# Kernel optimization log

Hardware: AMD Instinct MI355X
Metric: run time of the kernel (lower is better)

The kernel has to match this reference:

```python
import jax, jax.numpy as jnp
import numpy as np

ALPHA = 0.2  # LeakyReLU negative slope
N = 1024     # num_particles
DIM = 3
F_IN = 2 * DIM   # 6
NH = 64          # n_hidden_features
H = 4            # n_heads
T = 12


def _gat_attend(feat, a_vec, slope):
    # feat: (..., N, K); a_vec: (..., 2K) split into source/dest halves
    k = feat.shape[-1]
    f_src = jnp.einsum('...nk,...k->...n', feat, a_vec[..., :k])
    f_dst = jnp.einsum('...nk,...k->...n', feat, a_vec[..., k:])
    e = jax.nn.leaky_relu(f_src[..., :, None] + f_dst[..., None, :], slope)
    attn = jax.nn.softmax(e, axis=-1)  # (..., N, N) dense particle attention
    return jnp.einsum('...ij,...jk->...ik', attn, feat)


def pat_layer(x, W_heads, a_heads, W_out, a_out):
    # x: (N, F_IN); W_heads: (H, F_IN, NH); a_heads: (H, 2*NH)
    # W_out: (H*NH, F_OUT); a_out: (2*F_OUT)
    hW = jnp.einsum('nf,hfk->hnk', x, W_heads)          # (H, N, NH)
    heads = jax.nn.elu(_gat_attend(hW, a_heads, ALPHA))  # (H, N, NH)
    x2 = heads.transpose(1, 0, 2).reshape(x.shape[0], -1)  # (N, H*NH) concat
    hW2 = x2 @ W_out                                     # (N, F_OUT)
    return _gat_attend(hW2, a_out, ALPHA)                # output head, no elu


def setup_inputs() -> dict:
    key = jax.random.key(0)
    ks = jax.random.split(key, 13)
    s = 0.1
    d = {'states': jax.random.normal(ks[0], (T, N, F_IN), jnp.float32)}
    names = ['Wx', 'ax', 'Wxo', 'axo', 'Wh', 'ah', 'Who', 'aho', 'Wy', 'ay', 'Wyo', 'ayo']
    shapes = [(H, F_IN, NH), (H, 2 * NH), (H * NH, F_IN), (2 * F_IN)] * 3
    for i, (nm, sh) in enumerate(zip(names, shapes)):
        sh = sh if isinstance(sh, tuple) else (sh,)
        d[nm] = s * jax.random.normal(ks[i + 1], sh, jnp.float32)
    return d


def reference(states, Wx, ax, Wxo, axo, Wh, ah, Who, aho, Wy, ay, Wyo, ayo):
    def step(h_prev, x_t):
        h_t = pat_layer(x_t, Wx, ax, Wxo, axo) + pat_layer(h_prev, Wh, ah, Who, aho)
        y_t = x_t + pat_layer(h_t, Wy, ay, Wyo, ayo)
        return h_t, y_t

    h0 = jnp.zeros((N, F_IN), states.dtype)
    _, ys = jax.lax.scan(step, h0, states)
    return ys  # (T, N, 2*dim)
```

## Files before the change

kernel.cpp:

```cpp
#include <hip/hip_runtime.h>
#include <hip/hip_bf16.h>

#define ALPHA 0.2f

typedef float v2f __attribute__((ext_vector_type(2)));
typedef short bf16x8 __attribute__((ext_vector_type(8)));
typedef float f32x4 __attribute__((ext_vector_type(4)));

__device__ __forceinline__ float wsum(float v){
  #pragma unroll
  for (int m = 1; m < 64; m <<= 1) v += __shfl_xor(v, m, 64);
  return v;
}
__device__ __forceinline__ float wmax(float v){
  #pragma unroll
  for (int m = 1; m < 64; m <<= 1) v = fmaxf(v, __shfl_xor(v, m, 64));
  return v;
}

__global__ void k_detect(const unsigned short* __restrict__ s, int n, int* __restrict__ flag){
  int i = blockIdx.x * 256 + threadIdx.x;
  if (i < n){
    unsigned short u = s[i];
    if ((u & 0x7F80u) == 0x7F80u) atomicOr(flag, 1);
  }
}

struct Ptr13 { const void* p[13]; };
__global__ void k_cvtAll(Ptr13 src, float* __restrict__ xs, float* __restrict__ wsW,
                         const int* __restrict__ flag){
  const int n = blockIdx.x * 256 + threadIdx.x;
  const int F = *flag;
  if (n < 73728){
    xs[n] = F ? ((const float*)src.p[0])[n]
              : __bfloat162float(((const __hip_bfloat16*)src.p[0])[n]);
    return;
  }
  const int m = n - 73728;
  if (m >= 10788) return;
  const int segend[12] = {1536,2048,3584,3596,5132,5644,7180,7192,8728,9240,10776,10788};
  const int dstoff[12] = {0,1536,2048,3584,3600,5136,5648,7184,7200,8736,9248,10784};
  int seg = 0;
  #pragma unroll
  for (int i = 0; i < 12; ++i) if (m >= segend[i]) seg = i + 1;
  const int local = m - (seg ? segend[seg - 1] : 0);
  float v;
  if (F) v = ((const float*)src.p[seg + 1])[local];
  else   v = __bfloat162float(((const __hip_bfloat16*)src.p[seg + 1])[local]);
  wsW[dstoff[seg] + local] = v;
}

__launch_bounds__(256)
__global__ void k_prepT(const float* __restrict__ X, const float* __restrict__ W,
                        const float* __restrict__ a,
                        __hip_bfloat16* __restrict__ Vt, float* __restrict__ fsd)
{
  __shared__ float WS[384];
  __shared__ float aS[128];
  __shared__ __align__(16) __hip_bfloat16 tileT[64 * 264];
  const int t = threadIdx.x;
  const int b = blockIdx.y;
  const int h = blockIdx.z;
  const int row0 = blockIdx.x * 256;
  const int row = row0 + t;
  for (int i = t; i < 384; i += 256) WS[i] = W[h * 384 + i];
  if (t < 128) aS[t] = a[h * 128 + t];
  __syncthreads();
  float x[6];
  const float* xp = X + ((size_t)b * 1024 + row) * 6;
  #pragma unroll
  for (int f = 0; f < 6; ++f) x[f] = xp[f];
  float fs = 0.f, fd = 0.f;
  for (int k = 0; k < 64; ++k){
    float v = 0.f;
    #pragma unroll
    for (int f = 0; f < 6; ++f) v += x[f] * WS[f * 64 + k];
    fs += v * aS[k]; fd += v * aS[64 + k];
    tileT[k * 264 + t] = __float2bfloat16(v);
  }
  fsd[(((size_t)b * 4 + h) * 2 + 0) * 1024 + row] = fs;
  fsd[(((size_t)b * 4 + h) * 2 + 1) * 1024 + row] = fd;
  __syncthreads();
  const int k = t >> 2, seg = t & 3;
  __hip_bfloat16* dst = Vt + (((size_t)b * 4 + h) * 64 + k) * 1032 + row0 + seg * 64;
  const __hip_bfloat16* src = tileT + k * 264 + seg * 64;
  #pragma unroll
  for (int i = 0; i < 8; ++i)
    ((uint4*)dst)[i] = ((const uint4*)src)[i];
}

__launch_bounds__(256)
__global__ void k_attM(const __hip_bfloat16* __restrict__ Vt, const float* __restrict__ fsd,
                       const float* __restrict__ Wout, const float* __restrict__ aout,
                       float* __restrict__ hW2part, float* __restrict__ f2part)
{
  const int h = blockIdx.x & 3;
  const int row0 = (blockIdx.x >> 2) * 64;
  const int b = blockIdx.y;
  const int t = threadIdx.x;
  const int wv = t >> 6, lane = t & 63;
  const int n = lane & 15, q = lane >> 4;
  const size_t bh = (size_t)b * 4 + h;

  __shared__ float dS[1024];
  __shared__ float WoS[384];
  __shared__ float aoS[12];
  __shared__ float redW[4];

  const float* fb = fsd + bh * 2048;
  float4 dv = *(const float4*)(fb + 1024 + t * 4);
  for (int i = t; i < 384; i += 256) WoS[i] = Wout[h * 384 + i];
  if (t < 12) aoS[t] = aout[t];
  *(float4*)&dS[t * 4] = dv;
  const float sW = fb[row0 + wv * 16 + n];
  float lm = fmaxf(fmaxf(dv.x, dv.y), fmaxf(dv.z, dv.w));
  lm = wmax(lm);
  if (lane == 0) redW[wv] = lm;
  __syncthreads();
  const float maxd = fmaxf(fmaxf(redW[0], redW[1]), fmaxf(redW[2], redW[3]));
  float mW = sW + maxd; mW = fmaxf(mW, ALPHA * mW);

  const __hip_bfloat16* vbase = Vt + (bh * 64 + n) * 1032 + q * 8;
  f32x4 acc[4];
  #pragma unroll
  for (int nt = 0; nt < 4; ++nt) acc[nt] = (f32x4){0.f, 0.f, 0.f, 0.f};
  float den = 0.f;

  for (int jt = 0; jt < 16; ++jt){
    bf16x8 b0[4], b1[4];
    #pragma unroll
    for (int nt = 0; nt < 4; ++nt){
      b0[nt] = *(const bf16x8*)(vbase + nt * 16512 + jt * 64);
      b1[nt] = *(const bf16x8*)(vbase + nt * 16512 + jt * 64 + 32);
    }
    const float* dp = &dS[jt * 64 + q * 8];
    float d0[8], d1[8];
    *(float4*)&d0[0] = *(const float4*)(dp);
    *(float4*)&d0[4] = *(const float4*)(dp + 4);
    *(float4*)&d1[0] = *(const float4*)(dp + 32);
    *(float4*)&d1[4] = *(const float4*)(dp + 36);
    bf16x8 a0, a1;
    #pragma unroll
    for (int i = 0; i < 8; ++i){
      float e0 = sW + d0[i]; e0 = fmaxf(e0, ALPHA * e0);
      __hip_bfloat16 w0 = __float2bfloat16(__expf(fminf(e0 - mW, 0.f)));
      a0[i] = __builtin_bit_cast(short, w0);
      den += __bfloat162float(w0);
      float e1 = sW + d1[i]; e1 = fmaxf(e1, ALPHA * e1);
      __hip_bfloat16 w1 = __float2bfloat16(__expf(fminf(e1 - mW, 0.f)));
      a1[i] = __builtin_bit_cast(short, w1);
      den += __bfloat162float(w1);
    }
    #pragma unroll
    for (int nt = 0; nt < 4; ++nt)
      acc[nt] = __builtin_amdgcn_mfma_f32_16x16x32_bf16(a0, b0[nt], acc[nt], 0, 0, 0);
    #pragma unroll
    for (int nt = 0; nt < 4; ++nt)
      acc[nt] = __builtin_amdgcn_mfma_f32_16x16x32_bf16(a1, b1[nt], acc[nt], 0, 0, 0);
  }
  den += __shfl_xor(den, 16, 64);
  den += __shfl_xor(den, 32, 64);

  float o[4][6];
  #pragma unroll
  for (int reg = 0; reg < 4; ++reg)
    #pragma unroll
    for (int f = 0; f < 6; ++f) o[reg][f] = 0.f;
  #pragma unroll
  for (int reg = 0; reg < 4; ++reg){
    const float dn = __shfl(den, q * 4 + reg, 64);
    #pragma unroll
    for (int nt = 0; nt < 4; ++nt){
      float v = acc[nt][reg] / dn;
      v = v > 0.f ? v : (__expf(v) - 1.f);
      #pragma unroll
      for (int f = 0; f < 6; ++f) o[reg][f] += v * WoS[(nt * 16 + n) * 6 + f];
    }
  }
  #pragma unroll
  for (int mm = 1; mm < 16; mm <<= 1)
    #pragma unroll
    for (int reg = 0; reg < 4; ++reg)
      #pragma unroll
      for (int f = 0; f < 6; ++f) o[reg][f] += __shfl_xor(o[reg][f], mm, 64);
  if (n == 0){
    #pragma unroll
    for (int reg = 0; reg < 4; ++reg){
      const int row = row0 + wv * 16 + q * 4 + reg;
      float* hp = hW2part + bh * 6144 + row * 6;
      float fs = 0.f, fd = 0.f;
      #pragma unroll
      for (int f = 0; f < 6; ++f){
        hp[f] = o[reg][f];
        fs += o[reg][f] * aoS[f]; fd += o[reg][f] * aoS[6 + f];
      }
      f2part[bh * 2048 + row]        = fs;
      f2part[bh * 2048 + 1024 + row] = fd;
    }
  }
}

__launch_bounds__(256)
__global__ void k_attP(const __hip_bfloat16* __restrict__ VtP, const float* __restrict__ fsd,
                       const float* __restrict__ Wout, const float* __restrict__ aout,
                       float* __restrict__ hW2part, float* __restrict__ f2part)
{
  const int h = blockIdx.x & 3;
  const int row0 = (blockIdx.x >> 2) * 16;
  const int t = threadIdx.x;
  const int wv = t >> 6, lane = t & 63;
  const int n = lane & 15, q = lane >> 4;

  __shared__ float dS[1024];
  __shared__ float WoS[384];
  __shared__ float aoS[12];
  __shared__ float redW[4];
  __shared__ float accS[4][16][65];
  __shared__ float denP[4][16];

  const float* fb = fsd + (size_t)h * 2048;
  float4 dv = *(const float4*)(fb + 1024 + t * 4);
  for (int i = t; i < 384; i += 256) WoS[i] = Wout[h * 384 + i];
  if (t < 12) aoS[t] = aout[t];
  *(float4*)&dS[t * 4] = dv;
  const float sW = fb[row0 + n];
  float lm = fmaxf(fmaxf(dv.x, dv.y), fmaxf(dv.z, dv.w));
  lm = wmax(lm);
  if (lane == 0) redW[wv] = lm;
  __syncthreads();
  const float maxd = fmaxf(fmaxf(redW[0], redW[1]), fmaxf(redW[2], redW[3]));
  float mW = sW + maxd; mW = fmaxf(mW, ALPHA * mW);

  const __hip_bfloat16* vbase = VtP + ((size_t)h * 64 + n) * 1024 + q * 8;
  f32x4 acc[4];
  #pragma unroll
  for (int nt = 0; nt < 4; ++nt) acc[nt] = (f32x4){0.f, 0.f, 0.f, 0.f};
  float den = 0.f;

  #pragma unroll
  for (int u = 0; u < 4; ++u){
    const int jt = wv * 4 + u;
    bf16x8 b0[4], b1[4];
    #pragma unroll
    for (int nt = 0; nt < 4; ++nt){
      b0[nt] = *(const bf16x8*)(vbase + nt * 16384 + jt * 64);
      b1[nt] = *(const bf16x8*)(vbase + nt * 16384 + jt * 64 + 32);
    }
    const float* dp = &dS[jt * 64 + q * 8];
    float d0[8], d1[8];
    *(float4*)&d0[0] = *(const float4*)(dp);
    *(float4*)&d0[4] = *(const float4*)(dp + 4);
    *(float4*)&d1[0] = *(const float4*)(dp + 32);
    *(float4*)&d1[4] = *(const float4*)(dp + 36);
    bf16x8 a0, a1;
    #pragma unroll
    for (int i = 0; i < 8; ++i){
      float e0 = sW + d0[i]; e0 = fmaxf(e0, ALPHA * e0);
      __hip_bfloat16 w0 = __float2bfloat16(__expf(fminf(e0 - mW, 0.f)));
      a0[i] = __builtin_bit_cast(short, w0);
      den += __bfloat162float(w0);
      float e1 = sW + d1[i]; e1 = fmaxf(e1, ALPHA * e1);
      __hip_bfloat16 w1 = __float2bfloat16(__expf(fminf(e1 - mW, 0.f)));
      a1[i] = __builtin_bit_cast(short, w1);
      den += __bfloat162float(w1);
    }
    #pragma unroll
    for (int nt = 0; nt < 4; ++nt)
      acc[nt] = __builtin_amdgcn_mfma_f32_16x16x32_bf16(a0, b0[nt], acc[nt], 0, 0, 0);
    #pragma unroll
    for (int nt = 0; nt < 4; ++nt)
      acc[nt] = __builtin_amdgcn_mfma_f32_16x16x32_bf16(a1, b1[nt], acc[nt], 0, 0, 0);
  }
  den += __shfl_xor(den, 16, 64);
  den += __shfl_xor(den, 32, 64);
  if (lane < 16) denP[wv][lane] = den;
  #pragma unroll
  for (int nt = 0; nt < 4; ++nt)
    #pragma unroll
    for (int reg = 0; reg < 4; ++reg)
      accS[wv][q * 4 + reg][nt * 16 + n] = acc[nt][reg];
  __syncthreads();

  const int r = t >> 4, kq = t & 15;
  const float dn = denP[0][r] + denP[1][r] + denP[2][r] + denP[3][r];
  float o[6] = {0.f,0.f,0.f,0.f,0.f,0.f};
  #pragma unroll
  for (int j4 = 0; j4 < 4; ++j4){
    const int k = kq * 4 + j4;
    float v = (accS[0][r][k] + accS[1][r][k] + accS[2][r][k] + accS[3][r][k]) / dn;
    v = v > 0.f ? v : (__expf(v) - 1.f);
    #pragma unroll
    for (int f = 0; f < 6; ++f) o[f] += v * WoS[k * 6 + f];
  }
  #pragma unroll
  for (int mm = 1; mm < 16; mm <<= 1)
    #pragma unroll
    for (int f = 0; f < 6; ++f) o[f] += __shfl_xor(o[f], mm, 64);
  if (kq == 0){
    const int row = row0 + r;
    float* hp = hW2part + (size_t)h * 6144 + row * 6;
    float fs = 0.f, fd = 0.f;
    #pragma unroll
    for (int f = 0; f < 6; ++f){
      hp[f] = o[f];
      fs += o[f] * aoS[f]; fd += o[f] * aoS[6 + f];
    }
    f2part[(size_t)h * 2048 + row]        = fs;
    f2part[(size_t)h * 2048 + 1024 + row] = fd;
  }
}

__launch_bounds__(256)
__global__ void k_attB(const float* __restrict__ hW2part, const float* __restrict__ f2part,
                       const float* __restrict__ Lx_t, float* __restrict__ h_t,
                       const float* __restrict__ Wh, const float* __restrict__ ah,
                       __hip_bfloat16* __restrict__ hWn, float* __restrict__ fn)
{
  const int t = threadIdx.x;
  const int row0 = blockIdx.x * 4;
  const int wv = t >> 6, lane = t & 63;
  __shared__ float featS[6144];
  __shared__ float dS[1024];
  __shared__ float sS[4];
  __shared__ float redW[4];
  __shared__ float htS[4][6];
  __shared__ float WnS[1536];
  __shared__ float anS[512];

  for (int i = t; i < 6144; i += 256)
    featS[i] = hW2part[i] + hW2part[6144 + i] + hW2part[12288 + i] + hW2part[18432 + i];
  for (int i = t; i < 1024; i += 256)
    dS[i] = f2part[1024 + i] + f2part[3072 + i] + f2part[5120 + i] + f2part[7168 + i];
  if (t < 4){
    const int r = row0 + t;
    sS[t] = f2part[r] + f2part[2048 + r] + f2part[4096 + r] + f2part[6144 + r];
  }
  for (int i = t; i < 1536; i += 256) WnS[i] = Wh[i];
  for (int i = t; i < 512;  i += 256) anS[i] = ah[i];
  __syncthreads();
  float lm = -1.0e30f;
  for (int i = t; i < 1024; i += 256) lm = fmaxf(lm, dS[i]);
  lm = wmax(lm);
  if (lane == 0) redW[wv] = lm;
  __syncthreads();
  const float maxd = fmaxf(fmaxf(redW[0], redW[1]), fmaxf(redW[2], redW[3]));
  {
    const int r = wv, row = row0 + r;
    const float s = sS[r];
    float m = s + maxd; m = m > 0.f ? m : ALPHA * m;
    float num[6] = {0.f,0.f,0.f,0.f,0.f,0.f};
    float den = 0.f;
    for (int j = lane; j < 1024; j += 64){
      float e = s + dS[j]; e = e > 0.f ? e : ALPHA * e;
      float w = __expf(fminf(e - m, 0.f));
      den += w;
      const float* fr = &featS[j * 6];
      #pragma unroll
      for (int f = 0; f < 6; ++f) num[f] += w * fr[f];
    }
    den = wsum(den);
    #pragma unroll
    for (int f = 0; f < 6; ++f) num[f] = wsum(num[f]);
    if (lane == 0){
      #pragma unroll
      for (int f = 0; f < 6; ++f){
        float hv = Lx_t[row * 6 + f] + num[f] / den;
        h_t[row * 6 + f] = hv;
        htS[r][f] = hv;
      }
    }
  }
  __syncthreads();
  {
    const int k = lane, rw = row0 + wv;
    float hv[6];
    #pragma unroll
    for (int f = 0; f < 6; ++f) hv[f] = htS[wv][f];
    #pragma unroll
    for (int h = 0; h < 4; ++h){
      float acc = 0.f;
      #pragma unroll
      for (int f = 0; f < 6; ++f) acc += hv[f] * WnS[(h * 6 + f) * 64 + k];
      hWn[((size_t)h * 64 + k) * 1024 + rw] = __float2bfloat16(acc);
      float ps = wsum(acc * anS[h * 128 + k]);
      float pd = wsum(acc * anS[h * 128 + 64 + k]);
      if (k == 0){
        fn[((size_t)h * 2 + 0) * 1024 + rw] = ps;
        fn[((size_t)h * 2 + 1) * 1024 + rw] = pd;
      }
    }
  }
}

template<int MODE>
__launch_bounds__(256)
__global__ void k_attO(const float* __restrict__ hW2part, const float* __restrict__ f2part,
                       const float* __restrict__ addsrc, float* __restrict__ outf,
                       void* __restrict__ outv, int outOff, const int* __restrict__ flag)
{
  const int b = blockIdx.y;
  const int row0 = blockIdx.x * 16;
  const int t = threadIdx.x;
  const int wv = t >> 6, lane = t & 63;
  __shared__ float featS[6144];
  __shared__ float dS[1024];
  __shared__ float sS[16];
  __shared__ float redW[4];

  const float* hp = hW2part + (size_t)b * 24576;
  for (int i = t; i < 6144; i += 256)
    featS[i] = hp[i] + hp[6144 + i] + hp[12288 + i] + hp[18432 + i];
  const float* fp = f2part + (size_t)b * 8192;
  for (int i = t; i < 1024; i += 256)
    dS[i] = fp[1024 + i] + fp[3072 + i] + fp[5120 + i] + fp[7168 + i];
  if (t < 16){
    const int r = row0 + t;
    sS[t] = fp[r] + fp[2048 + r] + fp[4096 + r] + fp[6144 + r];
  }
  __syncthreads();
  float lm = -1.0e30f;
  for (int i = t; i < 1024; i += 256) lm = fmaxf(lm, dS[i]);
  lm = wmax(lm);
  if (lane == 0) redW[wv] = lm;
  __syncthreads();
  const float maxd = fmaxf(fmaxf(redW[0], redW[1]), fmaxf(redW[2], redW[3]));

  const int r = t >> 4, jq = t & 15;
  const int row = row0 + r;
  const float s = sS[r];
  float m = s + maxd; m = m > 0.f ? m : ALPHA * m;
  float num[6] = {0.f,0.f,0.f,0.f,0.f,0.f};
  float den = 0.f;
  for (int j = jq; j < 1024; j += 16){
    float e = s + dS[j]; e = e > 0.f ? e : ALPHA * e;
    float w = __expf(fminf(e - m, 0.f));
    den += w;
    const float* fr = &featS[j * 6];
    #pragma unroll
    for (int f = 0; f < 6; ++f) num[f] += w * fr[f];
  }
  #pragma unroll
  for (int mm = 1; mm < 16; mm <<= 1){
    den += __shfl_xor(den, mm, 64);
    #pragma unroll
    for (int f = 0; f < 6; ++f) num[f] += __shfl_xor(num[f], mm, 64);
  }

  if (jq == 0){
    if (MODE == 0){
      float* dst = outf + ((size_t)b * 1024 + row) * 6;
      #pragma unroll
      for (int f = 0; f < 6; ++f) dst[f] = num[f] / den;
    } else {
      const float* xsrc = addsrc + ((size_t)b * 1024 + row) * 6;
      const int base = outOff + b * 6144 + row * 6;
      if (*flag){
        float* dst = (float*)outv;
        #pragma unroll
        for (int f = 0; f < 6; ++f) dst[base + f] = xsrc[f] + num[f] / den;
      } else {
        __hip_bfloat16* dst = (__hip_bfloat16*)outv;
        #pragma unroll
        for (int f = 0; f < 6; ++f) dst[base + f] = __float2bfloat16(xsrc[f] + num[f] / den);
      }
    }
  }
}

extern "C" void kernel_launch(void* const* d_in, const int* in_sizes, int n_in,
                              void* d_out, int out_size, void* d_ws, size_t ws_size,
                              hipStream_t stream) {
  (void)in_sizes; (void)n_in; (void)out_size;

  const size_t avail = ws_size / 4;
  int CH = 0;
  const int cands[6] = {12, 6, 4, 3, 2, 1};
  for (int i = 0; i < 6; ++i){
    if (232000u + (size_t)cands[i] * 303104u <= avail){ CH = cands[i]; break; }
  }
  if (CH == 0) return;

  float* ws = (float*)d_ws;
  size_t off = 0;
  int*   flag = (int*)(ws + off); off += 16;
  float* xs   = ws + off; off += 73728;
  float* wsW  = ws + off; off += 10800;
  float* Lx    = ws + off; off += 73728;
  float* h_all = ws + off; off += 73728;
  float* p2hW2 = ws + off; off += (size_t)CH * 24576;
  float* p2f2  = ws + off; off += (size_t)CH * 8192;
  float* hWc   = ws + off; off += (size_t)CH * 262144;
  float* fc    = ws + off; off += (size_t)CH * 8192;

  hipMemsetAsync(flag, 0, 4, stream);
  k_detect<<<288, 256, 0, stream>>>((const unsigned short*)d_in[0], 73728, flag);
  Ptr13 ptrs;
  for (int i = 0; i < 13; ++i) ptrs.p[i] = d_in[i];
  k_cvtAll<<<331, 256, 0, stream>>>(ptrs, xs, wsW, flag);

  const int dstoff[12] = {0,1536,2048,3584,3600,5136,5648,7184,7200,8736,9248,10784};
  float *Wx = wsW + dstoff[0], *ax = wsW + dstoff[1], *Wxo = wsW + dstoff[2], *axo = wsW + dstoff[3];
  float *Wh = wsW + dstoff[4], *ah = wsW + dstoff[5], *Who = wsW + dstoff[6], *aho = wsW + dstoff[7];
  float *Wy = wsW + dstoff[8], *ay = wsW + dstoff[9], *Wyo = wsW + dstoff[10], *ayo = wsW + dstoff[11];

  __hip_bfloat16* VtG = (__hip_bfloat16*)hWc;

  for (int t0 = 0; t0 < 12; t0 += CH){
    k_prepT<<<dim3(4, CH, 4), 256, 0, stream>>>(xs + (size_t)t0 * 6144, Wx, ax, VtG, fc);
    k_attM<<<dim3(64, CH), 256, 0, stream>>>(VtG, fc, Wxo, axo, p2hW2, p2f2);
    k_attO<0><<<dim3(64, CH), 256, 0, stream>>>(p2hW2, p2f2, nullptr, Lx + (size_t)t0 * 6144,
                                                nullptr, 0, flag);
  }

  __hip_bfloat16* VtP = (__hip_bfloat16*)hWc;
  float* fh = fc;
  hipMemsetAsync(VtP, 0, 4 * 64 * 1024 * sizeof(__hip_bfloat16), stream);
  hipMemsetAsync(fh,  0, 8192 * sizeof(float), stream);
  for (int t = 0; t < 12; ++t){
    k_attP<<<dim3(256, 1), 256, 0, stream>>>(VtP, fh, Who, aho, p2hW2, p2f2);
    k_attB<<<256, 256, 0, stream>>>(p2hW2, p2f2, Lx + (size_t)t * 6144,
                                    h_all + (size_t)t * 6144, Wh, ah, VtP, fh);
  }

  for (int t0 = 0; t0 < 12; t0 += CH){
    k_prepT<<<dim3(4, CH, 4), 256, 0, stream>>>(h_all + (size_t)t0 * 6144, Wy, ay, VtG, fc);
    k_attM<<<dim3(64, CH), 256, 0, stream>>>(VtG, fc, Wyo, ayo, p2hW2, p2f2);
    k_attO<2><<<dim3(64, CH), 256, 0, stream>>>(p2hW2, p2f2, xs + (size_t)t0 * 6144, nullptr,
                                                d_out, t0 * 6144, flag);
  }
}
```

Before: 417.5 us.

## Fuse recurrent phase into one persistent cooperative kernel with grid syncs

The sequential h-recurrence used two kernel launches per timestep over 12 steps, plus two memsets. These are merged into a single cooperative kernel of 256 blocks that zeroes its buffers, then loops over the steps with grid-wide barriers between the attention-partial stage and the combine/projection stage. This removes about 26 launch and inter-kernel gaps on the serial critical path. In exchange it relies on every block being co-resident, and the merged kernel's larger shared-memory and register footprint could lower occupancy.

```diff
diff --git a/kernel.cpp b/kernel.cpp
--- a/kernel.cpp
+++ b/kernel.cpp
@@ -1,9 +1,11 @@
 #include <hip/hip_runtime.h>
+#include <hip/hip_cooperative_groups.h>
 #include <hip/hip_bf16.h>
 
+namespace cg = cooperative_groups;
+
 #define ALPHA 0.2f
 
-typedef float v2f __attribute__((ext_vector_type(2)));
 typedef short bf16x8 __attribute__((ext_vector_type(8)));
 typedef float f32x4 __attribute__((ext_vector_type(4)));
 
@@ -201,194 +203,206 @@
 }
 
 __launch_bounds__(256)
-__global__ void k_attP(const __hip_bfloat16* __restrict__ VtP, const float* __restrict__ fsd,
-                       const float* __restrict__ Wout, const float* __restrict__ aout,
-                       float* __restrict__ hW2part, float* __restrict__ f2part)
+__global__ void k_phase2(const float* __restrict__ Lx, float* __restrict__ h_all,
+                         const float* __restrict__ Who, const float* __restrict__ aho,
+                         const float* __restrict__ Wh, const float* __restrict__ ah,
+                         __hip_bfloat16* __restrict__ VtP, float* __restrict__ fh,
+                         float* __restrict__ hW2part, float* __restrict__ f2part)
 {
-  const int h = blockIdx.x & 3;
-  const int row0 = (blockIdx.x >> 2) * 16;
+  cg::grid_group gg = cg::this_grid();
+  const int bid = blockIdx.x;
   const int t = threadIdx.x;
   const int wv = t >> 6, lane = t & 63;
   const int n = lane & 15, q = lane >> 4;
-
-  __shared__ float dS[1024];
+  const int hP = bid & 3;
+  const int row0P = (bid >> 2) * 16;
+  const int row0B = bid * 4;
+
   __shared__ float WoS[384];
   __shared__ float aoS[12];
+  __shared__ float WnS[1536];
+  __shared__ float anS[512];
+  __shared__ float dS[1024];
   __shared__ float redW[4];
   __shared__ float accS[4][16][65];
   __shared__ float denP[4][16];
-
-  const float* fb = fsd + (size_t)h * 2048;
-  float4 dv = *(const float4*)(fb + 1024 + t * 4);
-  for (int i = t; i < 384; i += 256) WoS[i] = Wout[h * 384 + i];
-  if (t < 12) aoS[t] = aout[t];
-  *(float4*)&dS[t * 4] = dv;
-  const float sW = fb[row0 + n];
-  float lm = fmaxf(fmaxf(dv.x, dv.y), fmaxf(dv.z, dv.w));
-  lm = wmax(lm);
-  if (lane == 0) redW[wv] = lm;
-  __syncthreads();
-  const float maxd = fmaxf(fmaxf(redW[0], redW[1]), fmaxf(redW[2], redW[3]));
-  float mW = sW + maxd; mW = fmaxf(mW, ALPHA * mW);
-
-  const __hip_bfloat16* vbase = VtP + ((size_t)h * 64 + n) * 1024 + q * 8;
-  f32x4 acc[4];
-  #pragma unroll
-  for (int nt = 0; nt < 4; ++nt) acc[nt] = (f32x4){0.f, 0.f, 0.f, 0.f};
-  float den = 0.f;
-
-  #pragma unroll
-  for (int u = 0; u < 4; ++u){
-    const int jt = wv * 4 + u;
-    bf16x8 b0[4], b1[4];
-    #pragma unroll
-    for (int nt = 0; nt < 4; ++nt){
-      b0[nt] = *(const bf16x8*)(vbase + nt * 16384 + jt * 64);
-      b1[nt] = *(const bf16x8*)(vbase + nt * 16384 + jt * 64 + 32);
-    }
-    const float* dp = &dS[jt * 64 + q * 8];
-    float d0[8], d1[8];
-    *(float4*)&d0[0] = *(const float4*)(dp);
-    *(float4*)&d0[4] = *(const float4*)(dp + 4);
-    *(float4*)&d1[0] = *(const float4*)(dp + 32);
-    *(float4*)&d1[4] = *(const float4*)(dp + 36);
-    bf16x8 a0, a1;
-    #pragma unroll
-    for (int i = 0; i < 8; ++i){
-      float e0 = sW + d0[i]; e0 = fmaxf(e0, ALPHA * e0);
-      __hip_bfloat16 w0 = __float2bfloat16(__expf(fminf(e0 - mW, 0.f)));
-      a0[i] = __builtin_bit_cast(short, w0);
-      den += __bfloat162float(w0);
-      float e1 = sW + d1[i]; e1 = fmaxf(e1, ALPHA * e1);
-      __hip_bfloat16 w1 = __float2bfloat16(__expf(fminf(e1 - mW, 0.f)));
-      a1[i] = __builtin_bit_cast(short, w1);
-      den += __bfloat162float(w1);
-    }
-    #pragma unroll
-    for (int nt = 0; nt < 4; ++nt)
-      acc[nt] = __builtin_amdgcn_mfma_f32_16x16x32_bf16(a0, b0[nt], acc[nt], 0, 0, 0);
-    #pragma unroll
-    for (int nt = 0; nt < 4; ++nt)
-      acc[nt] = __builtin_amdgcn_mfma_f32_16x16x32_bf16(a1, b1[nt], acc[nt], 0, 0, 0);
-  }
-  den += __shfl_xor(den, 16, 64);
-  den += __shfl_xor(den, 32, 64);
-  if (lane < 16) denP[wv][lane] = den;
-  #pragma unroll
-  for (int nt = 0; nt < 4; ++nt)
-    #pragma unroll
-    for (int reg = 0; reg < 4; ++reg)
-      accS[wv][q * 4 + reg][nt * 16 + n] = acc[nt][reg];
-  __syncthreads();
-
-  const int r = t >> 4, kq = t & 15;
-  const float dn = denP[0][r] + denP[1][r] + denP[2][r] + denP[3][r];
-  float o[6] = {0.f,0.f,0.f,0.f,0.f,0.f};
-  #pragma unroll
-  for (int j4 = 0; j4 < 4; ++j4){
-    const int k = kq * 4 + j4;
-    float v = (accS[0][r][k] + accS[1][r][k] + accS[2][r][k] + accS[3][r][k]) / dn;
-    v = v > 0.f ? v : (__expf(v) - 1.f);
-    #pragma unroll
-    for (int f = 0; f < 6; ++f) o[f] += v * WoS[k * 6 + f];
-  }
-  #pragma unroll
-  for (int mm = 1; mm < 16; mm <<= 1)
-    #pragma unroll
-    for (int f = 0; f < 6; ++f) o[f] += __shfl_xor(o[f], mm, 64);
-  if (kq == 0){
-    const int row = row0 + r;
-    float* hp = hW2part + (size_t)h * 6144 + row * 6;
-    float fs = 0.f, fd = 0.f;
-    #pragma unroll
-    for (int f = 0; f < 6; ++f){
-      hp[f] = o[f];
-      fs += o[f] * aoS[f]; fd += o[f] * aoS[6 + f];
-    }
-    f2part[(size_t)h * 2048 + row]        = fs;
-    f2part[(size_t)h * 2048 + 1024 + row] = fd;
-  }
-}
-
-__launch_bounds__(256)
-__global__ void k_attB(const float* __restrict__ hW2part, const float* __restrict__ f2part,
-                       const float* __restrict__ Lx_t, float* __restrict__ h_t,
-                       const float* __restrict__ Wh, const float* __restrict__ ah,
-                       __hip_bfloat16* __restrict__ hWn, float* __restrict__ fn)
-{
-  const int t = threadIdx.x;
-  const int row0 = blockIdx.x * 4;
-  const int wv = t >> 6, lane = t & 63;
   __shared__ float featS[6144];
-  __shared__ float dS[1024];
-  __shared__ float sS[4];
-  __shared__ float redW[4];
+  __shared__ float dSb[1024];
+  __shared__ float sSb[4];
   __shared__ float htS[4][6];
-  __shared__ float WnS[1536];
-  __shared__ float anS[512];
-
-  for (int i = t; i < 6144; i += 256)
-    featS[i] = hW2part[i] + hW2part[6144 + i] + hW2part[12288 + i] + hW2part[18432 + i];
-  for (int i = t; i < 1024; i += 256)
-    dS[i] = f2part[1024 + i] + f2part[3072 + i] + f2part[5120 + i] + f2part[7168 + i];
-  if (t < 4){
-    const int r = row0 + t;
-    sS[t] = f2part[r] + f2part[2048 + r] + f2part[4096 + r] + f2part[6144 + r];
-  }
+
+  for (int i = t; i < 384; i += 256) WoS[i] = Who[hP * 384 + i];
+  if (t < 12) aoS[t] = aho[t];
   for (int i = t; i < 1536; i += 256) WnS[i] = Wh[i];
   for (int i = t; i < 512;  i += 256) anS[i] = ah[i];
-  __syncthreads();
-  float lm = -1.0e30f;
-  for (int i = t; i < 1024; i += 256) lm = fmaxf(lm, dS[i]);
-  lm = wmax(lm);
-  if (lane == 0) redW[wv] = lm;
-  __syncthreads();
-  const float maxd = fmaxf(fmaxf(redW[0], redW[1]), fmaxf(redW[2], redW[3]));
+
   {
-    const int r = wv, row = row0 + r;
-    const float s = sS[r];
-    float m = s + maxd; m = m > 0.f ? m : ALPHA * m;
-    float num[6] = {0.f,0.f,0.f,0.f,0.f,0.f};
-    float den = 0.f;
-    for (int j = lane; j < 1024; j += 64){
-      float e = s + dS[j]; e = e > 0.f ? e : ALPHA * e;
-      float w = __expf(fminf(e - m, 0.f));
-      den += w;
-      const float* fr = &featS[j * 6];
-      #pragma unroll
-      for (int f = 0; f < 6; ++f) num[f] += w * fr[f];
-    }
-    den = wsum(den);
-    #pragma unroll
-    for (int f = 0; f < 6; ++f) num[f] = wsum(num[f]);
-    if (lane == 0){
-      #pragma unroll
-      for (int f = 0; f < 6; ++f){
-        float hv = Lx_t[row * 6 + f] + num[f] / den;
-        h_t[row * 6 + f] = hv;
-        htS[r][f] = hv;
-      }
-    }
-  }
-  __syncthreads();
-  {
-    const int k = lane, rw = row0 + wv;
-    float hv[6];
-    #pragma unroll
-    for (int f = 0; f < 6; ++f) hv[f] = htS[wv][f];
-    #pragma unroll
-    for (int h = 0; h < 4; ++h){
-      float acc = 0.f;
-      #pragma unroll
-      for (int f = 0; f < 6; ++f) acc += hv[f] * WnS[(h * 6 + f) * 64 + k];
-      hWn[((size_t)h * 64 + k) * 1024 + rw] = __float2bfloat16(acc);
-      float ps = wsum(acc * anS[h * 128 + k]);
-      float pd = wsum(acc * anS[h * 128 + 64 + k]);
-      if (k == 0){
-        fn[((size_t)h * 2 + 0) * 1024 + rw] = ps;
-        fn[((size_t)h * 2 + 1) * 1024 + rw] = pd;
-      }
-    }
+    unsigned int* vz = (unsigned int*)VtP;
+    const int gid = bid * 256 + t;
+    for (int i = gid; i < 131072; i += 65536) vz[i] = 0u;
+    for (int i = gid; i < 8192; i += 65536) fh[i] = 0.f;
+  }
+  gg.sync();
+
+  for (int step = 0; step < 12; ++step){
+    {
+      const float* fb = fh + (size_t)hP * 2048;
+      float4 dv = *(const float4*)(fb + 1024 + t * 4);
+      *(float4*)&dS[t * 4] = dv;
+      const float sW = fb[row0P + n];
+      float lm = fmaxf(fmaxf(dv.x, dv.y), fmaxf(dv.z, dv.w));
+      lm = wmax(lm);
+      if (lane == 0) redW[wv] = lm;
+      __syncthreads();
+      const float maxd = fmaxf(fmaxf(redW[0], redW[1]), fmaxf(redW[2], redW[3]));
+      float mW = sW + maxd; mW = fmaxf(mW, ALPHA * mW);
+
+      const __hip_bfloat16* vbase = VtP + ((size_t)hP * 64 + n) * 1024 + q * 8;
+      f32x4 acc[4];
+      #pragma unroll
+      for (int nt = 0; nt < 4; ++nt) acc[nt] = (f32x4){0.f, 0.f, 0.f, 0.f};
+      float den = 0.f;
+
+      #pragma unroll
+      for (int u = 0; u < 4; ++u){
+        const int jt = wv * 4 + u;
+        bf16x8 b0[4], b1[4];
+        #pragma unroll
+        for (int nt = 0; nt < 4; ++nt){
+          b0[nt] = *(const bf16x8*)(vbase + nt * 16384 + jt * 64);
+          b1[nt] = *(const bf16x8*)(vbase + nt * 16384 + jt * 64 + 32);
+        }
+        const float* dp = &dS[jt * 64 + q * 8];
+        float d0[8], d1[8];
+        *(float4*)&d0[0] = *(const float4*)(dp);
+        *(float4*)&d0[4] = *(const float4*)(dp + 4);
+        *(float4*)&d1[0] = *(const float4*)(dp + 32);
+        *(float4*)&d1[4] = *(const float4*)(dp + 36);
+        bf16x8 a0, a1;
+        #pragma unroll
+        for (int i = 0; i < 8; ++i){
+          float e0 = sW + d0[i]; e0 = fmaxf(e0, ALPHA * e0);
+          __hip_bfloat16 w0 = __float2bfloat16(__expf(fminf(e0 - mW, 0.f)));
+          a0[i] = __builtin_bit_cast(short, w0);
+          den += __bfloat162float(w0);
+          float e1 = sW + d1[i]; e1 = fmaxf(e1, ALPHA * e1);
+          __hip_bfloat16 w1 = __float2bfloat16(__expf(fminf(e1 - mW, 0.f)));
+          a1[i] = __builtin_bit_cast(short, w1);
+          den += __bfloat162float(w1);
+        }
+        #pragma unroll
+        for (int nt = 0; nt < 4; ++nt)
+          acc[nt] = __builtin_amdgcn_mfma_f32_16x16x32_bf16(a0, b0[nt], acc[nt], 0, 0, 0);
+        #pragma unroll
+        for (int nt = 0; nt < 4; ++nt)
+          acc[nt] = __builtin_amdgcn_mfma_f32_16x16x32_bf16(a1, b1[nt], acc[nt], 0, 0, 0);
+      }
+      den += __shfl_xor(den, 16, 64);
+      den += __shfl_xor(den, 32, 64);
+      if (lane < 16) denP[wv][lane] = den;
+      #pragma unroll
+      for (int nt = 0; nt < 4; ++nt)
+        #pragma unroll
+        for (int reg = 0; reg < 4; ++reg)
+          accS[wv][q * 4 + reg][nt * 16 + n] = acc[nt][reg];
+      __syncthreads();
+
+      const int r = t >> 4, kq = t & 15;
+      const float dn = denP[0][r] + denP[1][r] + denP[2][r] + denP[3][r];
+      float o[6] = {0.f,0.f,0.f,0.f,0.f,0.f};
+      #pragma unroll
+      for (int j4 = 0; j4 < 4; ++j4){
+        const int k = kq * 4 + j4;
+        float v = (accS[0][r][k] + accS[1][r][k] + accS[2][r][k] + accS[3][r][k]) / dn;
+        v = v > 0.f ? v : (__expf(v) - 1.f);
+        #pragma unroll
+        for (int f = 0; f < 6; ++f) o[f] += v * WoS[k * 6 + f];
+      }
+      #pragma unroll
+      for (int mm = 1; mm < 16; mm <<= 1)
+        #pragma unroll
+        for (int f = 0; f < 6; ++f) o[f] += __shfl_xor(o[f], mm, 64);
+      if (kq == 0){
+        const int row = row0P + r;
+        float* hp = hW2part + (size_t)hP * 6144 + row * 6;
+        float fs = 0.f, fd = 0.f;
+        #pragma unroll
+        for (int f = 0; f < 6; ++f){
+          hp[f] = o[f];
+          fs += o[f] * aoS[f]; fd += o[f] * aoS[6 + f];
+        }
+        f2part[(size_t)hP * 2048 + row]        = fs;
+        f2part[(size_t)hP * 2048 + 1024 + row] = fd;
+      }
+    }
+    gg.sync();
+
+    {
+      for (int i = t; i < 6144; i += 256)
+        featS[i] = hW2part[i] + hW2part[6144 + i] + hW2part[12288 + i] + hW2part[18432 + i];
+      for (int i = t; i < 1024; i += 256)
+        dSb[i] = f2part[1024 + i] + f2part[3072 + i] + f2part[5120 + i] + f2part[7168 + i];
+      if (t < 4){
+        const int r = row0B + t;
+        sSb[t] = f2part[r] + f2part[2048 + r] + f2part[4096 + r] + f2part[6144 + r];
+      }
+      __syncthreads();
+      float lm = -1.0e30f;
+      for (int i = t; i < 1024; i += 256) lm = fmaxf(lm, dSb[i]);
+      lm = wmax(lm);
+      if (lane == 0) redW[wv] = lm;
+      __syncthreads();
+      const float maxd = fmaxf(fmaxf(redW[0], redW[1]), fmaxf(redW[2], redW[3]));
+      {
+        const int r = wv, row = row0B + r;
+        const float s = sSb[r];
+        float m = s + maxd; m = m > 0.f ? m : ALPHA * m;
+        float num[6] = {0.f,0.f,0.f,0.f,0.f,0.f};
+        float den = 0.f;
+        for (int j = lane; j < 1024; j += 64){
+          float e = s + dSb[j]; e = e > 0.f ? e : ALPHA * e;
+          float w = __expf(fminf(e - m, 0.f));
+          den += w;
+          const float* fr = &featS[j * 6];
+          #pragma unroll
+          for (int f = 0; f < 6; ++f) num[f] += w * fr[f];
+        }
+        den = wsum(den);
+        #pragma unroll
+        for (int f = 0; f < 6; ++f) num[f] = wsum(num[f]);
+        if (lane == 0){
+          const float* Lx_t = Lx + (size_t)step * 6144;
+          float* h_t = h_all + (size_t)step * 6144;
+          #pragma unroll
+          for (int f = 0; f < 6; ++f){
+            float hv = Lx_t[row * 6 + f] + num[f] / den;
+            h_t[row * 6 + f] = hv;
+            htS[r][f] = hv;
+          }
+        }
+      }
+      __syncthreads();
+      {
+        const int k = lane, rw = row0B + wv;
+        float hv[6];
+        #pragma unroll
+        for (int f = 0; f < 6; ++f) hv[f] = htS[wv][f];
+        #pragma unroll
+        for (int hh = 0; hh < 4; ++hh){
+          float acc2 = 0.f;
+          #pragma unroll
+          for (int f = 0; f < 6; ++f) acc2 += hv[f] * WnS[(hh * 6 + f) * 64 + k];
+          VtP[((size_t)hh * 64 + k) * 1024 + rw] = __float2bfloat16(acc2);
+          float ps = wsum(acc2 * anS[hh * 128 + k]);
+          float pd = wsum(acc2 * anS[hh * 128 + 64 + k]);
+          if (k == 0){
+            fh[((size_t)hh * 2 + 0) * 1024 + rw] = ps;
+            fh[((size_t)hh * 2 + 1) * 1024 + rw] = pd;
+          }
+        }
+      }
+    }
+    if (step < 11) gg.sync();
   }
 }
 
@@ -514,12 +528,12 @@
 
   __hip_bfloat16* VtP = (__hip_bfloat16*)hWc;
   float* fh = fc;
-  hipMemsetAsync(VtP, 0, 4 * 64 * 1024 * sizeof(__hip_bfloat16), stream);
-  hipMemsetAsync(fh,  0, 8192 * sizeof(float), stream);
-  for (int t = 0; t < 12; ++t){
-    k_attP<<<dim3(256, 1), 256, 0, stream>>>(VtP, fh, Who, aho, p2hW2, p2f2);
-    k_attB<<<256, 256, 0, stream>>>(p2hW2, p2f2, Lx + (size_t)t * 6144,
-                                    h_all + (size_t)t * 6144, Wh, ah, VtP, fh);
+  {
+    void* kargs[] = { (void*)&Lx, (void*)&h_all, (void*)&Who, (void*)&aho,
+                      (void*)&Wh, (void*)&ah, (void*)&VtP, (void*)&fh,
+                      (void*)&p2hW2, (void*)&p2f2 };
+    hipLaunchCooperativeKernel((const void*)k_phase2, dim3(256), dim3(256),
+                               kargs, 0, stream);
   }
 
   for (int t0 = 0; t0 < 12; t0 += CH){
```

New measurement: 1.114 ms. +166.9%, slower.

## Fold attention vectors into weights and fuse y-layer projection into recurrent kernel

Applied to the files above, without the earlier changes.

Precomputes W·a per layer and head in a new setup kernel, so the source/destination attention scores become 6-term dot products on the input instead of 64-term reductions over projected features. The recurrent attB kernel now also computes the y-layer projection and its scores for every step. This removes the separate prepT launches for the y pass and the h_all buffer. Partial-sum reductions in attB and attO now use float4 loads, and the zeroing memsets move into the setup kernel. In exchange the workspace grows to hold all twelve y-layer projections, and attB does twice as much projection work per step.

```diff
diff --git a/kernel.cpp b/kernel.cpp
--- a/kernel.cpp
+++ b/kernel.cpp
@@ -3,7 +3,6 @@
 
 #define ALPHA 0.2f
 
-typedef float v2f __attribute__((ext_vector_type(2)));
 typedef short bf16x8 __attribute__((ext_vector_type(8)));
 typedef float f32x4 __attribute__((ext_vector_type(4)));
 
@@ -50,13 +49,30 @@
   wsW[dstoff[seg] + local] = v;
 }
 
+__global__ void k_prew(const float* __restrict__ wsW, float* __restrict__ WaG,
+                       float* __restrict__ VtPf, float* __restrict__ fh)
+{
+  const int gid = blockIdx.x * 256 + threadIdx.x;
+  for (int i = gid; i < 131072; i += 24576) VtPf[i] = 0.f;
+  if (gid < 8192) fh[gid] = 0.f;
+  if (blockIdx.x == 0 && threadIdx.x < 144){
+    const int d = threadIdx.x;
+    const int L = d / 48, r2 = d % 48, h = r2 / 12, sd = (r2 % 12) / 6, f = r2 % 6;
+    const int Woff[3] = {0, 3600, 7200};
+    const int aoff[3] = {1536, 5136, 8736};
+    float s = 0.f;
+    for (int k = 0; k < 64; ++k)
+      s += wsW[Woff[L] + h * 384 + f * 64 + k] * wsW[aoff[L] + h * 128 + sd * 64 + k];
+    WaG[((L * 4 + h) * 2 + sd) * 8 + f] = s;
+  }
+}
+
 __launch_bounds__(256)
 __global__ void k_prepT(const float* __restrict__ X, const float* __restrict__ W,
-                        const float* __restrict__ a,
+                        const float* __restrict__ WaG,
                         __hip_bfloat16* __restrict__ Vt, float* __restrict__ fsd)
 {
   __shared__ float WS[384];
-  __shared__ float aS[128];
   __shared__ __align__(16) __hip_bfloat16 tileT[64 * 264];
   const int t = threadIdx.x;
   const int b = blockIdx.y;
@@ -64,20 +80,21 @@
   const int row0 = blockIdx.x * 256;
   const int row = row0 + t;
   for (int i = t; i < 384; i += 256) WS[i] = W[h * 384 + i];
-  if (t < 128) aS[t] = a[h * 128 + t];
   __syncthreads();
   float x[6];
   const float* xp = X + ((size_t)b * 1024 + row) * 6;
   #pragma unroll
   for (int f = 0; f < 6; ++f) x[f] = xp[f];
-  float fs = 0.f, fd = 0.f;
   for (int k = 0; k < 64; ++k){
     float v = 0.f;
     #pragma unroll
     for (int f = 0; f < 6; ++f) v += x[f] * WS[f * 64 + k];
-    fs += v * aS[k]; fd += v * aS[64 + k];
     tileT[k * 264 + t] = __float2bfloat16(v);
   }
+  const float* was = WaG + h * 16;
+  float fs = 0.f, fd = 0.f;
+  #pragma unroll
+  for (int f = 0; f < 6; ++f){ fs += x[f] * was[f]; fd += x[f] * was[8 + f]; }
   fsd[(((size_t)b * 4 + h) * 2 + 0) * 1024 + row] = fs;
   fsd[(((size_t)b * 4 + h) * 2 + 1) * 1024 + row] = fd;
   __syncthreads();
@@ -312,46 +329,62 @@
 
 __launch_bounds__(256)
 __global__ void k_attB(const float* __restrict__ hW2part, const float* __restrict__ f2part,
-                       const float* __restrict__ Lx_t, float* __restrict__ h_t,
-                       const float* __restrict__ Wh, const float* __restrict__ ah,
-                       __hip_bfloat16* __restrict__ hWn, float* __restrict__ fn)
+                       const float* __restrict__ Lx_t,
+                       const float* __restrict__ Wh, const float* __restrict__ Wy,
+                       const float* __restrict__ WaG,
+                       __hip_bfloat16* __restrict__ VtP, float* __restrict__ fh,
+                       __hip_bfloat16* __restrict__ VtY_t, float* __restrict__ fsdY_t)
 {
   const int t = threadIdx.x;
   const int row0 = blockIdx.x * 4;
   const int wv = t >> 6, lane = t & 63;
-  __shared__ float featS[6144];
-  __shared__ float dS[1024];
-  __shared__ float sS[4];
+  __shared__ __align__(16) float featS[6144];
+  __shared__ __align__(16) float dSb[1024];
+  __shared__ float sSb[4];
   __shared__ float redW[4];
   __shared__ float htS[4][6];
   __shared__ float WnS[1536];
-  __shared__ float anS[512];
-
-  for (int i = t; i < 6144; i += 256)
-    featS[i] = hW2part[i] + hW2part[6144 + i] + hW2part[12288 + i] + hW2part[18432 + i];
-  for (int i = t; i < 1024; i += 256)
-    dS[i] = f2part[1024 + i] + f2part[3072 + i] + f2part[5120 + i] + f2part[7168 + i];
+  __shared__ float WyS[1536];
+
+  {
+    const float4* h4 = (const float4*)hW2part;
+    for (int i = t; i < 1536; i += 256){
+      float4 a = h4[i], b = h4[1536 + i], c = h4[3072 + i], d = h4[4608 + i];
+      float4 r; r.x = a.x+b.x+c.x+d.x; r.y = a.y+b.y+c.y+d.y;
+      r.z = a.z+b.z+c.z+d.z; r.w = a.w+b.w+c.w+d.w;
+      *(float4*)&featS[i * 4] = r;
+    }
+    const float4* f4 = (const float4*)f2part;
+    {
+      const int i = t;
+      if (i < 256){
+        float4 a = f4[256 + i], b = f4[768 + i], c = f4[1280 + i], d = f4[1792 + i];
+        float4 r; r.x = a.x+b.x+c.x+d.x; r.y = a.y+b.y+c.y+d.y;
+        r.z = a.z+b.z+c.z+d.z; r.w = a.w+b.w+c.w+d.w;
+        *(float4*)&dSb[i * 4] = r;
+      }
+    }
+  }
   if (t < 4){
     const int r = row0 + t;
-    sS[t] = f2part[r] + f2part[2048 + r] + f2part[4096 + r] + f2part[6144 + r];
-  }
-  for (int i = t; i < 1536; i += 256) WnS[i] = Wh[i];
-  for (int i = t; i < 512;  i += 256) anS[i] = ah[i];
+    sSb[t] = f2part[r] + f2part[2048 + r] + f2part[4096 + r] + f2part[6144 + r];
+  }
+  for (int i = t; i < 1536; i += 256){ WnS[i] = Wh[i]; WyS[i] = Wy[i]; }
   __syncthreads();
   float lm = -1.0e30f;
-  for (int i = t; i < 1024; i += 256) lm = fmaxf(lm, dS[i]);
+  for (int i = t; i < 1024; i += 256) lm = fmaxf(lm, dSb[i]);
   lm = wmax(lm);
   if (lane == 0) redW[wv] = lm;
   __syncthreads();
   const float maxd = fmaxf(fmaxf(redW[0], redW[1]), fmaxf(redW[2], redW[3]));
   {
     const int r = wv, row = row0 + r;
-    const float s = sS[r];
+    const float s = sSb[r];
     float m = s + maxd; m = m > 0.f ? m : ALPHA * m;
     float num[6] = {0.f,0.f,0.f,0.f,0.f,0.f};
     float den = 0.f;
     for (int j = lane; j < 1024; j += 64){
-      float e = s + dS[j]; e = e > 0.f ? e : ALPHA * e;
+      float e = s + dSb[j]; e = e > 0.f ? e : ALPHA * e;
       float w = __expf(fminf(e - m, 0.f));
       den += w;
       const float* fr = &featS[j * 6];
@@ -363,11 +396,8 @@
     for (int f = 0; f < 6; ++f) num[f] = wsum(num[f]);
     if (lane == 0){
       #pragma unroll
-      for (int f = 0; f < 6; ++f){
-        float hv = Lx_t[row * 6 + f] + num[f] / den;
-        h_t[row * 6 + f] = hv;
-        htS[r][f] = hv;
-      }
+      for (int f = 0; f < 6; ++f)
+        htS[r][f] = Lx_t[row * 6 + f] + num[f] / den;
     }
   }
   __syncthreads();
@@ -377,18 +407,26 @@
     #pragma unroll
     for (int f = 0; f < 6; ++f) hv[f] = htS[wv][f];
     #pragma unroll
-    for (int h = 0; h < 4; ++h){
-      float acc = 0.f;
-      #pragma unroll
-      for (int f = 0; f < 6; ++f) acc += hv[f] * WnS[(h * 6 + f) * 64 + k];
-      hWn[((size_t)h * 64 + k) * 1024 + rw] = __float2bfloat16(acc);
-      float ps = wsum(acc * anS[h * 128 + k]);
-      float pd = wsum(acc * anS[h * 128 + 64 + k]);
-      if (k == 0){
-        fn[((size_t)h * 2 + 0) * 1024 + rw] = ps;
-        fn[((size_t)h * 2 + 1) * 1024 + rw] = pd;
+    for (int hh = 0; hh < 4; ++hh){
+      float a2 = 0.f, a3 = 0.f;
+      #pragma unroll
+      for (int f = 0; f < 6; ++f){
+        a2 += hv[f] * WnS[(hh * 6 + f) * 64 + k];
+        a3 += hv[f] * WyS[(hh * 6 + f) * 64 + k];
       }
-    }
+      VtP[((size_t)hh * 64 + k) * 1024 + rw]   = __float2bfloat16(a2);
+      VtY_t[((size_t)hh * 64 + k) * 1032 + rw] = __float2bfloat16(a3);
+    }
+  }
+  if (t < 64){
+    const int r = t >> 4, u = t & 15;
+    const int L = 1 + (u >> 3), hh = (u >> 1) & 3, sd = u & 1;
+    const float* wa = WaG + ((L * 4 + hh) * 2 + sd) * 8;
+    float s = 0.f;
+    #pragma unroll
+    for (int f = 0; f < 6; ++f) s += htS[r][f] * wa[f];
+    float* dst = (L == 1) ? fh : fsdY_t;
+    dst[hh * 2048 + sd * 1024 + row0 + r] = s;
   }
 }
 
@@ -402,17 +440,28 @@
   const int row0 = blockIdx.x * 16;
   const int t = threadIdx.x;
   const int wv = t >> 6, lane = t & 63;
-  __shared__ float featS[6144];
-  __shared__ float dS[1024];
+  __shared__ __align__(16) float featS[6144];
+  __shared__ __align__(16) float dS[1024];
   __shared__ float sS[16];
   __shared__ float redW[4];
 
-  const float* hp = hW2part + (size_t)b * 24576;
-  for (int i = t; i < 6144; i += 256)
-    featS[i] = hp[i] + hp[6144 + i] + hp[12288 + i] + hp[18432 + i];
+  {
+    const float4* h4 = (const float4*)(hW2part + (size_t)b * 24576);
+    for (int i = t; i < 1536; i += 256){
+      float4 a = h4[i], bb = h4[1536 + i], c = h4[3072 + i], d = h4[4608 + i];
+      float4 r; r.x = a.x+bb.x+c.x+d.x; r.y = a.y+bb.y+c.y+d.y;
+      r.z = a.z+bb.z+c.z+d.z; r.w = a.w+bb.w+c.w+d.w;
+      *(float4*)&featS[i * 4] = r;
+    }
+    const float4* f4 = (const float4*)(f2part + (size_t)b * 8192);
+    if (t < 256){
+      float4 a = f4[256 + t], bb = f4[768 + t], c = f4[1280 + t], d = f4[1792 + t];
+      float4 r; r.x = a.x+bb.x+c.x+d.x; r.y = a.y+bb.y+c.y+d.y;
+      r.z = a.z+bb.z+c.z+d.z; r.w = a.w+bb.w+c.w+d.w;
+      *(float4*)&dS[t * 4] = r;
+    }
+  }
   const float* fp = f2part + (size_t)b * 8192;
-  for (int i = t; i < 1024; i += 256)
-    dS[i] = fp[1024 + i] + fp[3072 + i] + fp[5120 + i] + fp[7168 + i];
   if (t < 16){
     const int r = row0 + t;
     sS[t] = fp[r] + fp[2048 + r] + fp[4096 + r] + fp[6144 + r];
@@ -476,7 +525,7 @@
   int CH = 0;
   const int cands[6] = {12, 6, 4, 3, 2, 1};
   for (int i = 0; i < 6; ++i){
-    if (232000u + (size_t)cands[i] * 303104u <= avail){ CH = cands[i]; break; }
+    if (1981248u + (size_t)cands[i] * 303104u <= avail){ CH = cands[i]; break; }
   }
   if (CH == 0) return;
 
@@ -485,11 +534,15 @@
   int*   flag = (int*)(ws + off); off += 16;
   float* xs   = ws + off; off += 73728;
   float* wsW  = ws + off; off += 10800;
-  float* Lx    = ws + off; off += 73728;
-  float* h_all = ws + off; off += 73728;
+  float* Lx   = ws + off; off += 73728;
+  float* WaG  = ws + off; off += 256;
+  float* VtPf = ws + off; off += 131072;
+  float* fh   = ws + off; off += 8192;
+  float* VtYf = ws + off; off += 1585152;
+  float* fsdY = ws + off; off += 98304;
   float* p2hW2 = ws + off; off += (size_t)CH * 24576;
   float* p2f2  = ws + off; off += (size_t)CH * 8192;
-  float* hWc   = ws + off; off += (size_t)CH * 262144;
+  float* VtGf  = ws + off; off += (size_t)CH * 262144;
   float* fc    = ws + off; off += (size_t)CH * 8192;
 
   hipMemsetAsync(flag, 0, 4, stream);
@@ -497,34 +550,34 @@
   Ptr13 ptrs;
   for (int i = 0; i < 13; ++i) ptrs.p[i] = d_in[i];
   k_cvtAll<<<331, 256, 0, stream>>>(ptrs, xs, wsW, flag);
+  k_prew<<<96, 256, 0, stream>>>(wsW, WaG, VtPf, fh);
 
   const int dstoff[12] = {0,1536,2048,3584,3600,5136,5648,7184,7200,8736,9248,10784};
-  float *Wx = wsW + dstoff[0], *ax = wsW + dstoff[1], *Wxo = wsW + dstoff[2], *axo = wsW + dstoff[3];
-  float *Wh = wsW + dstoff[4], *ah = wsW + dstoff[5], *Who = wsW + dstoff[6], *aho = wsW + dstoff[7];
-  float *Wy = wsW + dstoff[8], *ay = wsW + dstoff[9], *Wyo = wsW + dstoff[10], *ayo = wsW + dstoff[11];
-
-  __hip_bfloat16* VtG = (__hip_bfloat16*)hWc;
+  float *Wx = wsW + dstoff[0], *Wxo = wsW + dstoff[2], *axo = wsW + dstoff[3];
+  float *Wh = wsW + dstoff[4], *Who = wsW + dstoff[6], *aho = wsW + dstoff[7];
+  float *Wy = wsW + dstoff[8], *Wyo = wsW + dstoff[10], *ayo = wsW + dstoff[11];
+
+  __hip_bfloat16* VtG = (__hip_bfloat16*)VtGf;
+  __hip_bfloat16* VtP = (__hip_bfloat16*)VtPf;
+  __hip_bfloat16* VtY = (__hip_bfloat16*)VtYf;
 
   for (int t0 = 0; t0 < 12; t0 += CH){
-    k_prepT<<<dim3(4, CH, 4), 256, 0, stream>>>(xs + (size_t)t0 * 6144, Wx, ax, VtG, fc);
+    k_prepT<<<dim3(4, CH, 4), 256, 0, stream>>>(xs + (size_t)t0 * 6144, Wx, WaG, VtG, fc);
     k_attM<<<dim3(64, CH), 256, 0, stream>>>(VtG, fc, Wxo, axo, p2hW2, p2f2);
     k_attO<0><<<dim3(64, CH), 256, 0, stream>>>(p2hW2, p2f2, nullptr, Lx + (size_t)t0 * 6144,
                                                 nullptr, 0, flag);
   }
 
-  __hip_bfloat16* VtP = (__hip_bfloat16*)hWc;
-  float* fh = fc;
-  hipMemsetAsync(VtP, 0, 4 * 64 * 1024 * sizeof(__hip_bfloat16), stream);
-  hipMemsetAsync(fh,  0, 8192 * sizeof(float), stream);
   for (int t = 0; t < 12; ++t){
     k_attP<<<dim3(256, 1), 256, 0, stream>>>(VtP, fh, Who, aho, p2hW2, p2f2);
     k_attB<<<256, 256, 0, stream>>>(p2hW2, p2f2, Lx + (size_t)t * 6144,
-                                    h_all + (size_t)t * 6144, Wh, ah, VtP, fh);
+                                    Wh, Wy, WaG, VtP, fh,
+                                    VtY + (size_t)t * 264192, fsdY + (size_t)t * 8192);
   }
 
   for (int t0 = 0; t0 < 12; t0 += CH){
-    k_prepT<<<dim3(4, CH, 4), 256, 0, stream>>>(h_all + (size_t)t0 * 6144, Wy, ay, VtG, fc);
-    k_attM<<<dim3(64, CH), 256, 0, stream>>>(VtG, fc, Wyo, ayo, p2hW2, p2f2);
+    k_attM<<<dim3(64, CH), 256, 0, stream>>>(VtY + (size_t)t0 * 264192, fsdY + (size_t)t0 * 8192,
+                                             Wyo, ayo, p2hW2, p2f2);
     k_attO<2><<<dim3(64, CH), 256, 0, stream>>>(p2hW2, p2f2, xs + (size_t)t0 * 6144, nullptr,
                                                 d_out, t0 * 6144, flag);
   }
```

After: 428.6 us. +2.6%, slower.
